# Kernel optimization log

Measured on AMD Instinct MI355X. Metric: run time of the kernel, lower is better.

Reference implementation:

```python
import jax, jax.numpy as jnp
import numpy as np

NUM_CHANS = 64
LAG = 5
HIDDEN = [32, 32]  # module appends a final 1-channel layer
BATCH = 16
T = 2048


def setup_inputs() -> dict:
    key = jax.random.key(0)
    ks = jax.random.split(key, 7)
    p, h0, h1 = NUM_CHANS, HIDDEN[0], HIDDEN[1]
    # Per-network weights stacked along leading axis n = num_series = p.
    # Xavier-ish scale for layer 0 (Conv1d(p, h0, lag)), default-ish for rest.
    s0 = float(np.sqrt(2.0 / (p * LAG + h0)))
    return {
        "X": jax.random.normal(ks[0], (BATCH, T, p), dtype=jnp.float32),
        "W0": jax.random.normal(ks[1], (p, h0, p, LAG), dtype=jnp.float32) * s0,
        "b0": jax.random.normal(ks[2], (p, h0), dtype=jnp.float32) * 0.01,
        "W1": jax.random.normal(ks[3], (p, h1, h0), dtype=jnp.float32) * float(np.sqrt(1.0 / h0)),
        "b1": jax.random.normal(ks[4], (p, h1), dtype=jnp.float32) * 0.01,
        "W2": jax.random.normal(ks[5], (p, 1, h1), dtype=jnp.float32) * float(np.sqrt(1.0 / h1)),
        "b2": jax.random.normal(ks[6], (p, 1), dtype=jnp.float32) * 0.01,
    }


def reference(X, W0, b0, W1, b1, W2, b2):
    # X: [B, T, p]. Each of n=p networks: Conv1d(p,h0,lag) -> ReLU -> Conv1d(h0,h1,1)
    # -> ReLU -> Conv1d(h1,1,1); outputs concatenated along last dim.
    lag = W0.shape[-1]
    Tout = X.shape[1] - lag + 1  # valid conv output length
    # Sliding windows: Xwin[b,t,c,l] = X[b, t+l, c]  -> [B, Tout, p, lag]
    Xwin = jnp.stack([X[:, l:l + Tout, :] for l in range(lag)], axis=-1)
    # Layer 0 across all n networks at once: [B, n, Tout, h0]
    h = jnp.einsum('btcl,nhcl->bnth', Xwin, W0) + b0[None, :, None, :]
    # 1x1 conv layers (per-network dense along channel dim)
    h = jax.nn.relu(h)
    h = jnp.einsum('bnti,noi->bnto', h, W1) + b1[None, :, None, :]
    h = jax.nn.relu(h)
    h = jnp.einsum('bnti,noi->bnto', h, W2) + b2[None, :, None, :]  # [B, n, Tout, 1]
    # concat along dim 2 of (batch, Tout, 1) per network -> (B, Tout, n)
    return jnp.transpose(h[..., 0], (0, 2, 1))
```

## Files before the change

### kernel.cpp

```cpp
#include <hip/hip_runtime.h>

#define NCH 64
#define LAG 5
#define H0 32
#define H1 32
#define TIN 2048
#define TOUT 2044
#define NBATCH 16

#define XSTRIDE 72

typedef __attribute__((ext_vector_type(8))) short short8;
typedef __attribute__((ext_vector_type(4))) short short4v;
typedef __attribute__((ext_vector_type(4))) float f32x4;

__device__ __forceinline__ unsigned short f2bf(float f) {
    unsigned u = __float_as_uint(f);
    u += 0x7fffu + ((u >> 16) & 1u);
    return (unsigned short)(u >> 16);
}

__device__ __forceinline__ unsigned pack2bf_relu(float a, float b) {
    unsigned ua = __float_as_uint(fmaxf(a, 0.0f));
    unsigned ub = __float_as_uint(fmaxf(b, 0.0f));
    ua += 0x7fffu + ((ua >> 16) & 1u);
    ub += 0x7fffu + ((ub >> 16) & 1u);
    return (ua >> 16) | (ub & 0xffff0000u);
}

__device__ __forceinline__ short4v pack4bf_relu(const f32x4& v) {
    union { short4v s; unsigned u[2]; } cv;
    cv.u[0] = pack2bf_relu(v[0], v[1]);
    cv.u[1] = pack2bf_relu(v[2], v[3]);
    return cv.s;
}

__global__ __launch_bounds__(256) void prep_w(
    const float* __restrict__ W0, unsigned short* __restrict__ W0b,
    const float* __restrict__ W1, unsigned short* __restrict__ W1b,
    const float* __restrict__ W2, unsigned short* __restrict__ W2b)
{
    const int bx = blockIdx.x;
    if (bx < 512) {
        int j = bx * 256 + threadIdx.x;
        int nh = j >> 6, c = j & 63;
        const float* src = W0 + (size_t)j * LAG;
        unsigned short* dst = W0b + nh * 320 + c;
        #pragma unroll
        for (int l = 0; l < LAG; ++l) dst[l * 64] = f2bf(src[l]);
    } else if (bx < 544) {
        int i = ((bx - 512) * 256 + threadIdx.x) * 8;
        float4 a = *(const float4*)(W1 + i);
        float4 b = *(const float4*)(W1 + i + 4);
        unsigned long long v0 = (unsigned long long)f2bf(a.x)
                              | ((unsigned long long)f2bf(a.y) << 16)
                              | ((unsigned long long)f2bf(a.z) << 32)
                              | ((unsigned long long)f2bf(a.w) << 48);
        unsigned long long v1 = (unsigned long long)f2bf(b.x)
                              | ((unsigned long long)f2bf(b.y) << 16)
                              | ((unsigned long long)f2bf(b.z) << 32)
                              | ((unsigned long long)f2bf(b.w) << 48);
        *(unsigned long long*)(W1b + i)     = v0;
        *(unsigned long long*)(W1b + i + 4) = v1;
    } else {
        int i = threadIdx.x * 8;
        float4 a = *(const float4*)(W2 + i);
        float4 b = *(const float4*)(W2 + i + 4);
        unsigned long long v0 = (unsigned long long)f2bf(a.x)
                              | ((unsigned long long)f2bf(a.y) << 16)
                              | ((unsigned long long)f2bf(a.z) << 32)
                              | ((unsigned long long)f2bf(a.w) << 48);
        unsigned long long v1 = (unsigned long long)f2bf(b.x)
                              | ((unsigned long long)f2bf(b.y) << 16)
                              | ((unsigned long long)f2bf(b.z) << 32)
                              | ((unsigned long long)f2bf(b.w) << 48);
        *(unsigned long long*)(W2b + i)     = v0;
        *(unsigned long long*)(W2b + i + 4) = v1;
    }
}

__global__ __launch_bounds__(256, 3) void mlp_mfma(
    const float* __restrict__ X,
    const unsigned short* __restrict__ W0b,
    const unsigned short* __restrict__ W1b,
    const unsigned short* __restrict__ W2b,
    const float* __restrict__ b0, const float* __restrict__ b1,
    const float* __restrict__ b2, float* __restrict__ out)
{
    __shared__ __align__(16) unsigned short xs[260 * XSTRIDE];
    __shared__ __align__(8)  unsigned short yt[256][4];

    const int tileid = blockIdx.x;
    const int ng     = blockIdx.y;
    const int b      = tileid >> 3;
    const int t0     = (tileid & 7) * 256;
    const int tid    = threadIdx.x;
    const int wave   = tid >> 6;
    const int lane   = tid & 63;
    const int quad   = lane >> 4;
    const int l15    = lane & 15;

    const float* src = X + ((size_t)(b * TIN + t0)) * NCH;
    const int rows = (t0 == 1792) ? 256 : 260;
    for (int s = tid; s < rows * 16; s += 256) {
        int r = s >> 4, seg = s & 15;
        float4 x = *(const float4*)(src + s * 4);
        unsigned long long v = (unsigned long long)f2bf(x.x)
                             | ((unsigned long long)f2bf(x.y) << 16)
                             | ((unsigned long long)f2bf(x.z) << 32)
                             | ((unsigned long long)f2bf(x.w) << 48);
        *(unsigned long long*)&xs[r * XSTRIDE + seg * 4] = v;
    }
    __syncthreads();

    const int n = ng * 4 + wave;
    short8 B0[10][2];
    const unsigned short* wp0 = W0b + (n * H0 + l15) * (NCH * LAG) + quad * 8;
    #pragma unroll
    for (int ks = 0; ks < 10; ++ks) {
        B0[ks][0] = *(const short8*)(wp0 + ks * 32);
        B0[ks][1] = *(const short8*)(wp0 + 16 * (NCH * LAG) + ks * 32);
    }
    short4v A1[2][2];
    #pragma unroll
    for (int of = 0; of < 2; ++of)
        #pragma unroll
        for (int kf = 0; kf < 2; ++kf)
            A1[of][kf] = *(const short4v*)(W1b + (n * H1 + of * 16 + l15) * H0 + kf * 16 + quad * 4);
    short4v A2[2];
    #pragma unroll
    for (int kf = 0; kf < 2; ++kf)
        A2[kf] = *(const short4v*)(W2b + n * H1 + kf * 16 + quad * 4);
    f32x4 b0q[2], b1q[2];
    #pragma unroll
    for (int nf = 0; nf < 2; ++nf) b0q[nf] = *(const f32x4*)(b0 + (size_t)n * H0 + nf * 16 + quad * 4);
    #pragma unroll
    for (int of = 0; of < 2; ++of) b1q[of] = *(const f32x4*)(b1 + (size_t)n * H1 + of * 16 + quad * 4);
    const float b2s = b2[n];

    const int vmax = (t0 == 1792) ? 251 : 255;

    #pragma unroll 1
    for (int chunk = 0; chunk < 8; ++chunk) {
        int rowoff[2];
        #pragma unroll
        for (int mf = 0; mf < 2; ++mf) {
            int i = chunk * 32 + mf * 16 + l15;
            i = i < vmax ? i : vmax;
            rowoff[mf] = i * XSTRIDE + quad * 8;
        }

        f32x4 acc[2][2];
        #pragma unroll
        for (int mf = 0; mf < 2; ++mf) {
            acc[mf][0] = b0q[0];
            acc[mf][1] = b0q[1];
        }
        #pragma unroll
        for (int ks = 0; ks < 10; ++ks) {
            const int xoff = (ks >> 1) * XSTRIDE + (ks & 1) * 32;
            #pragma unroll
            for (int mf = 0; mf < 2; ++mf) {
                short8 Xf = *(const short8*)&xs[rowoff[mf] + xoff];
                acc[mf][0] = __builtin_amdgcn_mfma_f32_16x16x32_bf16(B0[ks][0], Xf, acc[mf][0], 0, 0, 0);
                acc[mf][1] = __builtin_amdgcn_mfma_f32_16x16x32_bf16(B0[ks][1], Xf, acc[mf][1], 0, 0, 0);
            }
        }

        #pragma unroll
        for (int mf = 0; mf < 2; ++mf) {
            short4v Bh0 = pack4bf_relu(acc[mf][0]);
            short4v Bh1 = pack4bf_relu(acc[mf][1]);

            f32x4 D1[2] = { b1q[0], b1q[1] };
            D1[0] = __builtin_amdgcn_mfma_f32_16x16x16bf16_1k(A1[0][0], Bh0, D1[0], 0, 0, 0);
            D1[0] = __builtin_amdgcn_mfma_f32_16x16x16bf16_1k(A1[0][1], Bh1, D1[0], 0, 0, 0);
            D1[1] = __builtin_amdgcn_mfma_f32_16x16x16bf16_1k(A1[1][0], Bh0, D1[1], 0, 0, 0);
            D1[1] = __builtin_amdgcn_mfma_f32_16x16x16bf16_1k(A1[1][1], Bh1, D1[1], 0, 0, 0);

            short4v Bg0 = pack4bf_relu(D1[0]);
            short4v Bg1 = pack4bf_relu(D1[1]);

            f32x4 D2 = (f32x4){ b2s, b2s, b2s, b2s };
            D2 = __builtin_amdgcn_mfma_f32_16x16x16bf16_1k(A2[0], Bg0, D2, 0, 0, 0);
            D2 = __builtin_amdgcn_mfma_f32_16x16x16bf16_1k(A2[1], Bg1, D2, 0, 0, 0);

            if (quad == 0)
                yt[chunk * 32 + mf * 16 + l15][wave] = f2bf(D2[0]);
        }
    }
    __syncthreads();

    int t = t0 + tid;
    if (t < TOUT) {
        ushort4 v = *(const ushort4*)yt[tid];
        float4 o;
        o.x = __uint_as_float((unsigned)v.x << 16);
        o.y = __uint_as_float((unsigned)v.y << 16);
        o.z = __uint_as_float((unsigned)v.z << 16);
        o.w = __uint_as_float((unsigned)v.w << 16);
        *(float4*)&out[((size_t)(b * TOUT + t)) * NCH + ng * 4] = o;
    }
}

extern "C" void kernel_launch(void* const* d_in, const int* in_sizes, int n_in,
                              void* d_out, int out_size, void* d_ws, size_t ws_size,
                              hipStream_t stream)
{
    const float* X  = (const float*)d_in[0];
    const float* W0 = (const float*)d_in[1];
    const float* b0 = (const float*)d_in[2];
    const float* W1 = (const float*)d_in[3];
    const float* b1 = (const float*)d_in[4];
    const float* W2 = (const float*)d_in[5];
    const float* b2 = (const float*)d_in[6];
    float* out = (float*)d_out;

    unsigned short* W0b = (unsigned short*)d_ws;
    unsigned short* W1b = (unsigned short*)((char*)d_ws + 1310720);
    unsigned short* W2b = (unsigned short*)((char*)d_ws + 1441792);

    prep_w<<<545, 256, 0, stream>>>(W0, W0b, W1, W1b, W2, W2b);
    mlp_mfma<<<dim3(128, 16), 256, 0, stream>>>(X, W0b, W1b, W2b, b0, b1, b2, out);
}
```

Baseline: 126.6 us.

## Pre-convert X to padded bf16 and stage tiles via direct global-to-LDS loads

X is now converted to bf16 once, in a padded row layout, inside the prep kernel. Previously each of the 16 network-group blocks re-read the fp32 X tile and converted it itself. The main kernel copies the padded bf16 tile straight into LDS with global_load_lds and issues the weight register loads before the barrier, so those loads overlap the LDS fill. This cuts redundant fp32 reads and conversions, at the cost of an extra write and read of a roughly 4.7MB bf16 buffer. Reading 37KB per tile may run past the end of the buffer on the last tile.

```diff
diff --git a/kernel.cpp b/kernel.cpp
--- a/kernel.cpp
+++ b/kernel.cpp
@@ -35,21 +35,31 @@
     return cv.s;
 }
 
-__global__ __launch_bounds__(256) void prep_w(
+__global__ __launch_bounds__(256) void prep_all(
+    const float* __restrict__ X,  unsigned short* __restrict__ Xpad,
     const float* __restrict__ W0, unsigned short* __restrict__ W0b,
     const float* __restrict__ W1, unsigned short* __restrict__ W1b,
     const float* __restrict__ W2, unsigned short* __restrict__ W2b)
 {
     const int bx = blockIdx.x;
-    if (bx < 512) {
+    if (bx < 2048) {
         int j = bx * 256 + threadIdx.x;
+        int row = j >> 4, seg = j & 15;
+        float4 x = *(const float4*)(X + (size_t)j * 4);
+        unsigned long long v = (unsigned long long)f2bf(x.x)
+                             | ((unsigned long long)f2bf(x.y) << 16)
+                             | ((unsigned long long)f2bf(x.z) << 32)
+                             | ((unsigned long long)f2bf(x.w) << 48);
+        *(unsigned long long*)(Xpad + (size_t)row * XSTRIDE + seg * 4) = v;
+    } else if (bx < 2560) {
+        int j = (bx - 2048) * 256 + threadIdx.x;
         int nh = j >> 6, c = j & 63;
         const float* src = W0 + (size_t)j * LAG;
         unsigned short* dst = W0b + nh * 320 + c;
         #pragma unroll
         for (int l = 0; l < LAG; ++l) dst[l * 64] = f2bf(src[l]);
-    } else if (bx < 544) {
-        int i = ((bx - 512) * 256 + threadIdx.x) * 8;
+    } else if (bx < 2592) {
+        int i = ((bx - 2560) * 256 + threadIdx.x) * 8;
         float4 a = *(const float4*)(W1 + i);
         float4 b = *(const float4*)(W1 + i + 4);
         unsigned long long v0 = (unsigned long long)f2bf(a.x)
@@ -80,14 +90,14 @@
 }
 
 __global__ __launch_bounds__(256, 3) void mlp_mfma(
-    const float* __restrict__ X,
+    const unsigned short* __restrict__ Xpad,
     const unsigned short* __restrict__ W0b,
     const unsigned short* __restrict__ W1b,
     const unsigned short* __restrict__ W2b,
     const float* __restrict__ b0, const float* __restrict__ b1,
     const float* __restrict__ b2, float* __restrict__ out)
 {
-    __shared__ __align__(16) unsigned short xs[260 * XSTRIDE];
+    __shared__ __align__(16) unsigned short xs[37 * 512];
     __shared__ __align__(8)  unsigned short yt[256][4];
 
     const int tileid = blockIdx.x;
@@ -100,18 +110,16 @@
     const int quad   = lane >> 4;
     const int l15    = lane & 15;
 
-    const float* src = X + ((size_t)(b * TIN + t0)) * NCH;
-    const int rows = (t0 == 1792) ? 256 : 260;
-    for (int s = tid; s < rows * 16; s += 256) {
-        int r = s >> 4, seg = s & 15;
-        float4 x = *(const float4*)(src + s * 4);
-        unsigned long long v = (unsigned long long)f2bf(x.x)
-                             | ((unsigned long long)f2bf(x.y) << 16)
-                             | ((unsigned long long)f2bf(x.z) << 32)
-                             | ((unsigned long long)f2bf(x.w) << 48);
-        *(unsigned long long*)&xs[r * XSTRIDE + seg * 4] = v;
-    }
-    __syncthreads();
+    {
+        const char* srcb = (const char*)(Xpad + (size_t)(b * TIN + t0) * XSTRIDE);
+        #pragma unroll 1
+        for (int i = wave; i < 37; i += 4) {
+            __builtin_amdgcn_global_load_lds(
+                (const __attribute__((address_space(1))) unsigned int*)(srcb + i * 1024 + lane * 16),
+                (__attribute__((address_space(3))) unsigned int*)((char*)xs + i * 1024),
+                16, 0, 0);
+        }
+    }
 
     const int n = ng * 4 + wave;
     short8 B0[10][2];
@@ -137,6 +145,8 @@
     #pragma unroll
     for (int of = 0; of < 2; ++of) b1q[of] = *(const f32x4*)(b1 + (size_t)n * H1 + of * 16 + quad * 4);
     const float b2s = b2[n];
+
+    __syncthreads();
 
     const int vmax = (t0 == 1792) ? 251 : 255;
 
@@ -216,10 +226,11 @@
     const float* b2 = (const float*)d_in[6];
     float* out = (float*)d_out;
 
-    unsigned short* W0b = (unsigned short*)d_ws;
-    unsigned short* W1b = (unsigned short*)((char*)d_ws + 1310720);
-    unsigned short* W2b = (unsigned short*)((char*)d_ws + 1441792);
-
-    prep_w<<<545, 256, 0, stream>>>(W0, W0b, W1, W1b, W2, W2b);
-    mlp_mfma<<<dim3(128, 16), 256, 0, stream>>>(X, W0b, W1b, W2b, b0, b1, b2, out);
-}
+    unsigned short* Xpad = (unsigned short*)d_ws;
+    unsigned short* W0b  = (unsigned short*)((char*)d_ws + 4726784);
+    unsigned short* W1b  = (unsigned short*)((char*)d_ws + 6037504);
+    unsigned short* W2b  = (unsigned short*)((char*)d_ws + 6168576);
+
+    prep_all<<<2593, 256, 0, stream>>>(X, Xpad, W0, W0b, W1, W1b, W2, W2b);
+    mlp_mfma<<<dim3(128, 16), 256, 0, stream>>>(Xpad, W0b, W1b, W2b, b0, b1, b2, out);
+}
```

After: 122.5 us. 1.03x faster.
